# Kernel optimization log

Measured on AMD Instinct MI355X. Metric: run time of the kernel, lower is better.

Reference implementation:

```python
import jax, jax.numpy as jnp
import numpy as np

T, B = 1024, 64
IN, HID, OUT, ASZ = 512, 512, 512, 128


def lstm_cell(x, h, c, Wih, Whh, bih, bhh):
    g = x @ Wih.T + bih + h @ Whh.T + bhh
    i, f, gg, o = jnp.split(g, 4, axis=1)
    c2 = jax.nn.sigmoid(f) * c + jax.nn.sigmoid(i) * jnp.tanh(gg)
    h2 = jax.nn.sigmoid(o) * jnp.tanh(c2)
    return h2, c2


def arnn_cell(x, h, pol, Wih, Whh, b, ninp, nhid):
    # policy chunks: [ninp, nhid, nhid, nhid, nhid, nhid]
    p_in = pol[:, :ninp]
    p_h = pol[:, ninp:ninp + nhid]
    p_ig = pol[:, ninp + nhid:ninp + 2 * nhid]
    p_hg = pol[:, ninp + 2 * nhid:ninp + 3 * nhid]
    p_b = pol[:, ninp + 3 * nhid:ninp + 4 * nhid]
    ig = ((x * p_in) @ Wih.T) * p_ig + b * p_b
    hg = ((h * p_h) @ Whh.T) * p_hg
    return jnp.tanh(ig + hg)


def setup_inputs() -> dict:
    key = jax.random.key(0)
    ks = list(jax.random.split(key, 24))
    s = 0.1
    d = {"x": jax.random.normal(ks[0], (T, B, IN), dtype=jnp.float32)}
    # layer 0: ninp=IN, nhid=HID; layer 1: ninp=HID, nhid=OUT
    for l, (ninp, nhid) in enumerate([(IN, HID), (HID, OUT)]):
        ain = ASZ + ninp + nhid
        psz = ninp + 5 * nhid
        base = 1 + 9 * l
        d[f"aW_ih{l}"] = jax.random.normal(ks[base + 0], (4 * ASZ, ain)) * s
        d[f"aW_hh{l}"] = jax.random.normal(ks[base + 1], (4 * ASZ, ASZ)) * s
        d[f"ab_ih{l}"] = jax.random.normal(ks[base + 2], (4 * ASZ,)) * s
        d[f"ab_hh{l}"] = jax.random.normal(ks[base + 3], (4 * ASZ,)) * s
        d[f"pW{l}"] = jax.random.normal(ks[base + 4], (psz, ASZ)) * s
        d[f"pb{l}"] = jax.random.normal(ks[base + 5], (psz,)) * s
        d[f"fW_ih{l}"] = jax.random.normal(ks[base + 6], (nhid, ninp)) * s
        d[f"fW_hh{l}"] = jax.random.normal(ks[base + 7], (nhid, nhid)) * s
        d[f"fb{l}"] = jax.random.normal(ks[base + 8], (nhid,)) * s
    return d


def reference(x, aW_ih0, aW_hh0, ab_ih0, ab_hh0, pW0, pb0, fW_ih0, fW_hh0, fb0,
              aW_ih1, aW_hh1, ab_ih1, ab_hh1, pW1, pb1, fW_ih1, fW_hh1, fb1):
    zB = lambda n: jnp.zeros((B, n), dtype=x.dtype)
    init = (zB(ASZ), zB(ASZ), zB(ASZ), zB(ASZ), zB(HID), zB(OUT))

    def step(carry, xt):
        ahx0, ahc0, ahx1, ahc1, fhx0, fhx1 = carry
        # layer 0: adapt input = [x_t, fhx0, adapt_hx of layer -1 (= layer 1)]
        ax0 = jnp.concatenate([xt, fhx0, ahx1], axis=1)
        ahx0, ahc0 = lstm_cell(ax0, ahx0, ahc0, aW_ih0, aW_hh0, ab_ih0, ab_hh0)
        pol0 = ahx0 @ pW0.T + pb0
        fhx0 = arnn_cell(xt, fhx0, pol0, fW_ih0, fW_hh0, fb0, IN, HID)
        # layer 1
        ax1 = jnp.concatenate([fhx0, fhx1, ahx0], axis=1)
        ahx1, ahc1 = lstm_cell(ax1, ahx1, ahc1, aW_ih1, aW_hh1, ab_ih1, ab_hh1)
        pol1 = ahx1 @ pW1.T + pb1
        fhx1 = arnn_cell(fhx0, fhx1, pol1, fW_ih1, fW_hh1, fb1, HID, OUT)
        return (ahx0, ahc0, ahx1, ahc1, fhx0, fhx1), fhx1

    _, out = jax.lax.scan(step, init, x)  # out: [T, B, OUT]
    return out
```

## Files before the change

kernel.cpp:

```cpp
#include <hip/hip_runtime.h>

#define TT    1024
#define NTHR  512
#define NWG   256

#define XB_SZ  65536
#define XA0    0
#define XA1    2048
#define XF0    4096
#define XF1    12288
#define XP0    20480
#define XP1    40960
#define X_ZERO_END 20480

#define O_BARB (8 * XB_SZ)

__device__ __forceinline__ float sigm(float x) { return 1.f / (1.f + __expf(-x)); }

__device__ __forceinline__ float dot_ks(const float* __restrict__ a,
                                        const float* __restrict__ w,
                                        int nq, int ks) {
  float s0=0.f,s1=0.f,s2=0.f,s3=0.f;
  const float4* a4=(const float4*)a; const float4* w4=(const float4*)w;
  #pragma unroll 8
  for (int k = 0; k < nq; ++k) {
    int i4 = (k<<2) + ks;
    float4 av = a4[i4], wv = w4[i4];
    s0=fmaf(av.x,wv.x,s0); s1=fmaf(av.y,wv.y,s1);
    s2=fmaf(av.z,wv.z,s2); s3=fmaf(av.w,wv.w,s3);
  }
  return (s0+s1)+(s2+s3);
}
__device__ __forceinline__ float dot3_ks(const float* __restrict__ a,
                                         const float* __restrict__ pp,
                                         const float* __restrict__ w,
                                         int nq, int ks) {
  float s0=0.f,s1=0.f,s2=0.f,s3=0.f;
  const float4* a4=(const float4*)a; const float4* p4=(const float4*)pp;
  const float4* w4=(const float4*)w;
  #pragma unroll 8
  for (int k = 0; k < nq; ++k) {
    int i4 = (k<<2) + ks;
    float4 av = a4[i4], pv = p4[i4], wv = w4[i4];
    s0=fmaf(av.x*pv.x,wv.x,s0); s1=fmaf(av.y*pv.y,wv.y,s1);
    s2=fmaf(av.z*pv.z,wv.z,s2); s3=fmaf(av.w*pv.w,wv.w,s3);
  }
  return (s0+s1)+(s2+s3);
}
__device__ __forceinline__ float dot_full(const float* __restrict__ a,
                                          const float* __restrict__ w) {
  float s0=0.f,s1=0.f,s2=0.f,s3=0.f;
  const float4* a4=(const float4*)a; const float4* w4=(const float4*)w;
  #pragma unroll 8
  for (int k = 0; k < 32; ++k) {
    float4 av = a4[k], wv = w4[k];
    s0=fmaf(av.x,wv.x,s0); s1=fmaf(av.y,wv.y,s1);
    s2=fmaf(av.z,wv.z,s2); s3=fmaf(av.w,wv.w,s3);
  }
  return (s0+s1)+(s2+s3);
}

__device__ __forceinline__ void xbar(int* cnt, int* ep, int e, int tid) {
  __syncthreads();
  if (tid == 0) {
    int old = __hip_atomic_fetch_add(cnt, 1, __ATOMIC_RELAXED,
                                     __HIP_MEMORY_SCOPE_AGENT);
    if (old == e * 32 - 1)
      __hip_atomic_store(ep, e, __ATOMIC_RELAXED, __HIP_MEMORY_SCOPE_AGENT);
    while (__hip_atomic_load(ep, __ATOMIC_RELAXED,
                             __HIP_MEMORY_SCOPE_AGENT) < e)
      __builtin_amdgcn_s_sleep(1);
    (void)__hip_atomic_load(ep, __ATOMIC_ACQUIRE, __HIP_MEMORY_SCOPE_AGENT);
  }
  __syncthreads();
}

struct Params {
  const float* x;
  const float *aW_ih0, *aW_hh0, *ab_ih0, *ab_hh0, *pW0, *pb0, *fW_ih0, *fW_hh0, *fb0;
  const float *aW_ih1, *aW_hh1, *ab_ih1, *ab_hh1, *pW1, *pb1, *fW_ih1, *fW_hh1, *fb1;
  float* out;
  float* ws;
};

__global__ __launch_bounds__(NTHR, 1)
void arnn_kernel(Params p) {
  extern __shared__ float lds[];
  __shared__ int s_rank;
  const int tid = threadIdx.x;
  float* __restrict__ ws = p.ws;

  int xcd;
  asm volatile("s_getreg_b32 %0, hwreg(HW_REG_XCC_ID)" : "=s"(xcd));
  xcd &= 7;

  int* bar = (int*)(ws + O_BARB);
  if (tid == 0)
    s_rank = __hip_atomic_fetch_add(&bar[2048 + xcd], 1,
                                    __ATOMIC_RELAXED, __HIP_MEMORY_SCOPE_AGENT);
  __syncthreads();
  const int r = s_rank;
  int* cnt = &bar[xcd * 256];
  int* ep  = &bar[xcd * 256 + 64];

  float* xb = ws + (size_t)xcd * XB_SZ;
  const int b0 = xcd * 8;

  for (int i = r * NTHR + tid; i < X_ZERO_END; i += 32 * NTHR) xb[i] = 0.f;

  const int lane = tid & 63;
  const int ks   = tid & 3;
  const int jj = tid >> 7, blL = (tid >> 4) & 7, q = (tid >> 2) & 3;
  const int jL = r * 4 + jj;
  const bool cell = (tid & 15) == 0;
  const int c4 = tid >> 5, blA = (tid >> 2) & 7;
  const int cA = r * 16 + c4;
  const int nA = r * 80 + (tid >> 3), blP = tid & 7;
  const int nB = r * 80 + 64 + (tid >> 3);

  float bi0=0,bf0=0,bg0=0,bo0=0, bi1=0,bf1=0,bg1=0,bo1=0;
  if (cell) {
    bi0 = p.ab_ih0[0*128+jL] + p.ab_hh0[0*128+jL];
    bf0 = p.ab_ih0[1*128+jL] + p.ab_hh0[1*128+jL];
    bg0 = p.ab_ih0[2*128+jL] + p.ab_hh0[2*128+jL];
    bo0 = p.ab_ih0[3*128+jL] + p.ab_hh0[3*128+jL];
    bi1 = p.ab_ih1[0*128+jL] + p.ab_hh1[0*128+jL];
    bf1 = p.ab_ih1[1*128+jL] + p.ab_hh1[1*128+jL];
    bg1 = p.ab_ih1[2*128+jL] + p.ab_hh1[2*128+jL];
    bo1 = p.ab_ih1[3*128+jL] + p.ab_hh1[3*128+jL];
  }
  const float fb0c = p.fb0[cA], fb1c = p.fb1[cA];
  const float pb0a = p.pb0[nA], pb1a = p.pb1[nA];
  float pb0b = 0.f, pb1b = 0.f;
  if (tid < 128) { pb0b = p.pb0[nB]; pb1b = p.pb1[nB]; }

  const int rowL = q * 128 + jL;
  const float* wih0 = p.aW_ih0 + (size_t)rowL * 1152;
  const float* whh0 = p.aW_hh0 + (size_t)rowL * 128;
  const float* wih1 = p.aW_ih1 + (size_t)rowL * 1152;
  const float* whh1 = p.aW_hh1 + (size_t)rowL * 128;
  const float* fwi0 = p.fW_ih0 + (size_t)cA * 512;
  const float* fwh0 = p.fW_hh0 + (size_t)cA * 512;
  const float* fwi1 = p.fW_ih1 + (size_t)cA * 512;
  const float* fwh1 = p.fW_hh1 + (size_t)cA * 512;

  float creg0 = 0.f, creg1 = 0.f;

  int e = 1;
  xbar(cnt, ep, e, tid);

  for (int t = 0; t < TT; ++t) {
    const int old = t & 1, nw = old ^ 1;
    float* ahx0_o = xb + XA0 + old * 1024;
    float* ahx0_n = xb + XA0 + nw  * 1024;
    float* ahx1_o = xb + XA1 + old * 1024;
    float* ahx1_n = xb + XA1 + nw  * 1024;
    float* fhx0_o = xb + XF0 + old * 4096;
    float* fhx0_n = xb + XF0 + nw  * 4096;
    float* fhx1_o = xb + XF1 + old * 4096;
    float* fhx1_n = xb + XF1 + nw  * 4096;
    float* pol0   = xb + XP0;
    float* pol1   = xb + XP1;
    const float* xt = p.x + ((size_t)t * 64 + b0) * 512;

    {
      float s = dot_ks(xt     + blL * 512, wih0,        32, ks)
              + dot_ks(fhx0_o + blL * 512, wih0 + 512,  32, ks)
              + dot_ks(ahx1_o + blL * 128, wih0 + 1024,  8, ks)
              + dot_ks(ahx0_o + blL * 128, whh0,         8, ks);
      s += __shfl_xor(s, 1); s += __shfl_xor(s, 2);
      float gi = __shfl(s,(lane&48)+0),  gf = __shfl(s,(lane&48)+4);
      float gg = __shfl(s,(lane&48)+8),  go = __shfl(s,(lane&48)+12);
      if (cell) {
        gi += bi0; gf += bf0; gg += bg0; go += bo0;
        float c2 = sigm(gf) * creg0 + sigm(gi) * tanhf(gg);
        creg0 = c2;
        ahx0_n[blL * 128 + jL] = sigm(go) * tanhf(c2);
      }
    }
    ++e; xbar(cnt, ep, e, tid);

    {
      pol0[blP * 2560 + nA] = pb0a +
          dot_full(ahx0_n + blP * 128, p.pW0 + (size_t)nA * 128);
      if (tid < 128)
        pol0[blP * 2560 + nB] = pb0b +
            dot_full(ahx0_n + blP * 128, p.pW0 + (size_t)nB * 128);
    }
    ++e; xbar(cnt, ep, e, tid);

    {
      const float* pr = pol0 + blA * 2560;
      float sig = dot3_ks(xt     + blA * 512, pr,       fwi0, 32, ks);
      float shg = dot3_ks(fhx0_o + blA * 512, pr + 512, fwh0, 32, ks);
      sig += __shfl_xor(sig, 1); sig += __shfl_xor(sig, 2);
      shg += __shfl_xor(shg, 1); shg += __shfl_xor(shg, 2);
      if (ks == 0) {
        float v = tanhf(sig * pr[1024 + cA] + fb0c * pr[2048 + cA]
                      + shg * pr[1536 + cA]);
        fhx0_n[blA * 512 + cA] = v;
      }
    }
    ++e; xbar(cnt, ep, e, tid);

    {
      float s = dot_ks(fhx0_n + blL * 512, wih1,        32, ks)
              + dot_ks(fhx1_o + blL * 512, wih1 + 512,  32, ks)
              + dot_ks(ahx0_n + blL * 128, wih1 + 1024,  8, ks)
              + dot_ks(ahx1_o + blL * 128, whh1,         8, ks);
      s += __shfl_xor(s, 1); s += __shfl_xor(s, 2);
      float gi = __shfl(s,(lane&48)+0),  gf = __shfl(s,(lane&48)+4);
      float gg = __shfl(s,(lane&48)+8),  go = __shfl(s,(lane&48)+12);
      if (cell) {
        gi += bi1; gf += bf1; gg += bg1; go += bo1;
        float c2 = sigm(gf) * creg1 + sigm(gi) * tanhf(gg);
        creg1 = c2;
        ahx1_n[blL * 128 + jL] = sigm(go) * tanhf(c2);
      }
    }
    ++e; xbar(cnt, ep, e, tid);

    {
      pol1[blP * 2560 + nA] = pb1a +
          dot_full(ahx1_n + blP * 128, p.pW1 + (size_t)nA * 128);
      if (tid < 128)
        pol1[blP * 2560 + nB] = pb1b +
            dot_full(ahx1_n + blP * 128, p.pW1 + (size_t)nB * 128);
    }
    ++e; xbar(cnt, ep, e, tid);

    {
      const float* pr = pol1 + blA * 2560;
      float sig = dot3_ks(fhx0_n + blA * 512, pr,       fwi1, 32, ks);
      float shg = dot3_ks(fhx1_o + blA * 512, pr + 512, fwh1, 32, ks);
      sig += __shfl_xor(sig, 1); sig += __shfl_xor(sig, 2);
      shg += __shfl_xor(shg, 1); shg += __shfl_xor(shg, 2);
      if (ks == 0) {
        float v = tanhf(sig * pr[1024 + cA] + fb1c * pr[2048 + cA]
                      + shg * pr[1536 + cA]);
        fhx1_n[blA * 512 + cA] = v;
        p.out[((size_t)t * 64 + b0 + blA) * 512 + cA] = v;
      }
    }
    ++e; xbar(cnt, ep, e, tid);
  }
  (void)lds;
}

extern "C" void kernel_launch(void* const* d_in, const int* in_sizes, int n_in,
                              void* d_out, int out_size, void* d_ws, size_t ws_size,
                              hipStream_t stream) {
  Params prm;
  prm.x      = (const float*)d_in[0];
  prm.aW_ih0 = (const float*)d_in[1];
  prm.aW_hh0 = (const float*)d_in[2];
  prm.ab_ih0 = (const float*)d_in[3];
  prm.ab_hh0 = (const float*)d_in[4];
  prm.pW0    = (const float*)d_in[5];
  prm.pb0    = (const float*)d_in[6];
  prm.fW_ih0 = (const float*)d_in[7];
  prm.fW_hh0 = (const float*)d_in[8];
  prm.fb0    = (const float*)d_in[9];
  prm.aW_ih1 = (const float*)d_in[10];
  prm.aW_hh1 = (const float*)d_in[11];
  prm.ab_ih1 = (const float*)d_in[12];
  prm.ab_hh1 = (const float*)d_in[13];
  prm.pW1    = (const float*)d_in[14];
  prm.pb1    = (const float*)d_in[15];
  prm.fW_ih1 = (const float*)d_in[16];
  prm.fW_hh1 = (const float*)d_in[17];
  prm.fb1    = (const float*)d_in[18];
  prm.out    = (float*)d_out;
  prm.ws     = (float*)d_ws;

  hipMemsetAsync((char*)d_ws + (size_t)O_BARB * 4, 0, 16384, stream);

  static int lds_bytes = 84 * 1024;
  hipFuncSetAttribute((const void*)arnn_kernel,
                      hipFuncAttributeMaxDynamicSharedMemorySize, lds_bytes);

  void* kargs[] = { (void*)&prm };
  hipLaunchCooperativeKernel((const void*)arnn_kernel, dim3(NWG), dim3(NTHR),
                             kargs, lds_bytes, stream);
}
```

Baseline: 98.07 ms.

## Stage next phase's weights into double-buffered LDS overlapped with current compute

Each phase now issues global loads of the next phase's weight slice into registers, then computes from LDS, then writes the staged registers into the alternate LDS buffer before the grid barrier. Weight reads in the dot products come from padded LDS rows instead of global memory, and the global latency is hidden behind the current phase. This costs extra register pressure (nine float4 staging registers) and extra LDS write traffic on every phase, and the per-step weight reload from L2 still happens.

```diff
diff --git a/kernel.cpp b/kernel.cpp
--- a/kernel.cpp
+++ b/kernel.cpp
@@ -14,6 +14,8 @@
 #define X_ZERO_END 20480
 
 #define O_BARB (8 * XB_SZ)
+
+#define BUF_FL 18496
 
 __device__ __forceinline__ float sigm(float x) { return 1.f / (1.f + __expf(-x)); }
 
@@ -60,6 +62,60 @@
   return (s0+s1)+(s2+s3);
 }
 
+__device__ __forceinline__ void stg_lstm_ld(const float* Wih, int r, float4* st, int tid) {
+  const float4* g = (const float4*)Wih;
+  #pragma unroll
+  for (int k = 0; k < 9; ++k) {
+    int c = tid + k * 512;
+    int rr = c / 288, cq = c - rr * 288;
+    int grow = (rr >> 2) * 128 + r * 4 + (rr & 3);
+    st[k] = g[(size_t)grow * 288 + cq];
+  }
+}
+__device__ __forceinline__ void stg_lstm_wr(float* buf, const float4* st, int tid) {
+  #pragma unroll
+  for (int k = 0; k < 9; ++k) {
+    int c = tid + k * 512;
+    int rr = c / 288, cq = c - rr * 288;
+    *(float4*)(buf + rr * 1156 + cq * 4) = st[k];
+  }
+}
+__device__ __forceinline__ void stg_pol_ld(const float* pW, int r, float4* st, int tid) {
+  const float4* g = (const float4*)pW;
+  #pragma unroll
+  for (int k = 0; k < 5; ++k) {
+    int c = tid + k * 512;
+    int rw = c >> 5, cq = c & 31;
+    st[k] = g[(size_t)(r * 80 + rw) * 32 + cq];
+  }
+}
+__device__ __forceinline__ void stg_pol_wr(float* buf, const float4* st, int tid) {
+  #pragma unroll
+  for (int k = 0; k < 5; ++k) {
+    int c = tid + k * 512;
+    int rw = c >> 5, cq = c & 31;
+    *(float4*)(buf + rw * 132 + cq * 4) = st[k];
+  }
+}
+__device__ __forceinline__ void stg_arnn_ld(const float* Wih, const float* Whh,
+                                            int r, float4* st, int tid) {
+  #pragma unroll
+  for (int k = 0; k < 8; ++k) {
+    int c = tid + k * 512;
+    int rw = c >> 7, cq = c & 127;
+    const float4* g = (const float4*)((rw < 16) ? Wih : Whh);
+    st[k] = g[(size_t)(r * 16 + (rw & 15)) * 128 + cq];
+  }
+}
+__device__ __forceinline__ void stg_arnn_wr(float* buf, const float4* st, int tid) {
+  #pragma unroll
+  for (int k = 0; k < 8; ++k) {
+    int c = tid + k * 512;
+    int rw = c >> 7, cq = c & 127;
+    *(float4*)(buf + rw * 516 + cq * 4) = st[k];
+  }
+}
+
 __device__ __forceinline__ void xbar(int* cnt, int* ep, int e, int tid) {
   __syncthreads();
   if (tid == 0) {
@@ -115,8 +171,9 @@
   const bool cell = (tid & 15) == 0;
   const int c4 = tid >> 5, blA = (tid >> 2) & 7;
   const int cA = r * 16 + c4;
-  const int nA = r * 80 + (tid >> 3), blP = tid & 7;
-  const int nB = r * 80 + 64 + (tid >> 3);
+  const int nAr = tid >> 3, blP = tid & 7;
+  const int nA = r * 80 + nAr;
+  const int nB = r * 80 + 64 + nAr;
 
   float bi0=0,bf0=0,bg0=0,bo0=0, bi1=0,bf1=0,bg1=0,bo1=0;
   if (cell) {
@@ -135,16 +192,14 @@
   if (tid < 128) { pb0b = p.pb0[nB]; pb1b = p.pb1[nB]; }
 
   const int rowL = q * 128 + jL;
-  const float* wih0 = p.aW_ih0 + (size_t)rowL * 1152;
   const float* whh0 = p.aW_hh0 + (size_t)rowL * 128;
-  const float* wih1 = p.aW_ih1 + (size_t)rowL * 1152;
   const float* whh1 = p.aW_hh1 + (size_t)rowL * 128;
-  const float* fwi0 = p.fW_ih0 + (size_t)cA * 512;
-  const float* fwh0 = p.fW_hh0 + (size_t)cA * 512;
-  const float* fwi1 = p.fW_ih1 + (size_t)cA * 512;
-  const float* fwh1 = p.fW_hh1 + (size_t)cA * 512;
 
   float creg0 = 0.f, creg1 = 0.f;
+  float4 st[9];
+
+  stg_lstm_ld(p.aW_ih0, r, st, tid);
+  stg_lstm_wr(lds, st, tid);
 
   int e = 1;
   xbar(cnt, ep, e, tid);
@@ -163,11 +218,13 @@
     float* pol1   = xb + XP1;
     const float* xt = p.x + ((size_t)t * 64 + b0) * 512;
 
-    {
-      float s = dot_ks(xt     + blL * 512, wih0,        32, ks)
-              + dot_ks(fhx0_o + blL * 512, wih0 + 512,  32, ks)
-              + dot_ks(ahx1_o + blL * 128, wih0 + 1024,  8, ks)
-              + dot_ks(ahx0_o + blL * 128, whh0,         8, ks);
+    stg_pol_ld(p.pW0, r, st, tid);
+    {
+      const float* w = lds + (q * 4 + jj) * 1156;
+      float s = dot_ks(xt     + blL * 512, w,        32, ks)
+              + dot_ks(fhx0_o + blL * 512, w + 512,  32, ks)
+              + dot_ks(ahx1_o + blL * 128, w + 1024,  8, ks)
+              + dot_ks(ahx0_o + blL * 128, whh0,      8, ks);
       s += __shfl_xor(s, 1); s += __shfl_xor(s, 2);
       float gi = __shfl(s,(lane&48)+0),  gf = __shfl(s,(lane&48)+4);
       float gg = __shfl(s,(lane&48)+8),  go = __shfl(s,(lane&48)+12);
@@ -178,21 +235,26 @@
         ahx0_n[blL * 128 + jL] = sigm(go) * tanhf(c2);
       }
     }
-    ++e; xbar(cnt, ep, e, tid);
-
-    {
-      pol0[blP * 2560 + nA] = pb0a +
-          dot_full(ahx0_n + blP * 128, p.pW0 + (size_t)nA * 128);
+    stg_pol_wr(lds + BUF_FL, st, tid);
+    ++e; xbar(cnt, ep, e, tid);
+
+    stg_arnn_ld(p.fW_ih0, p.fW_hh0, r, st, tid);
+    {
+      const float* Lb = lds + BUF_FL;
+      pol0[blP * 2560 + nA] = pb0a + dot_full(ahx0_n + blP * 128, Lb + nAr * 132);
       if (tid < 128)
-        pol0[blP * 2560 + nB] = pb0b +
-            dot_full(ahx0_n + blP * 128, p.pW0 + (size_t)nB * 128);
-    }
-    ++e; xbar(cnt, ep, e, tid);
-
-    {
+        pol0[blP * 2560 + nB] = pb0b + dot_full(ahx0_n + blP * 128, Lb + (64 + nAr) * 132);
+    }
+    stg_arnn_wr(lds, st, tid);
+    ++e; xbar(cnt, ep, e, tid);
+
+    stg_lstm_ld(p.aW_ih1, r, st, tid);
+    {
+      const float* wi = lds + c4 * 516;
+      const float* wh = lds + (16 + c4) * 516;
       const float* pr = pol0 + blA * 2560;
-      float sig = dot3_ks(xt     + blA * 512, pr,       fwi0, 32, ks);
-      float shg = dot3_ks(fhx0_o + blA * 512, pr + 512, fwh0, 32, ks);
+      float sig = dot3_ks(xt     + blA * 512, pr,       wi, 32, ks);
+      float shg = dot3_ks(fhx0_o + blA * 512, pr + 512, wh, 32, ks);
       sig += __shfl_xor(sig, 1); sig += __shfl_xor(sig, 2);
       shg += __shfl_xor(shg, 1); shg += __shfl_xor(shg, 2);
       if (ks == 0) {
@@ -201,13 +263,16 @@
         fhx0_n[blA * 512 + cA] = v;
       }
     }
-    ++e; xbar(cnt, ep, e, tid);
-
-    {
-      float s = dot_ks(fhx0_n + blL * 512, wih1,        32, ks)
-              + dot_ks(fhx1_o + blL * 512, wih1 + 512,  32, ks)
-              + dot_ks(ahx0_n + blL * 128, wih1 + 1024,  8, ks)
-              + dot_ks(ahx1_o + blL * 128, whh1,         8, ks);
+    stg_lstm_wr(lds + BUF_FL, st, tid);
+    ++e; xbar(cnt, ep, e, tid);
+
+    stg_pol_ld(p.pW1, r, st, tid);
+    {
+      const float* w = lds + BUF_FL + (q * 4 + jj) * 1156;
+      float s = dot_ks(fhx0_n + blL * 512, w,        32, ks)
+              + dot_ks(fhx1_o + blL * 512, w + 512,  32, ks)
+              + dot_ks(ahx0_n + blL * 128, w + 1024,  8, ks)
+              + dot_ks(ahx1_o + blL * 128, whh1,      8, ks);
       s += __shfl_xor(s, 1); s += __shfl_xor(s, 2);
       float gi = __shfl(s,(lane&48)+0),  gf = __shfl(s,(lane&48)+4);
       float gg = __shfl(s,(lane&48)+8),  go = __shfl(s,(lane&48)+12);
@@ -218,21 +283,25 @@
         ahx1_n[blL * 128 + jL] = sigm(go) * tanhf(c2);
       }
     }
-    ++e; xbar(cnt, ep, e, tid);
-
-    {
-      pol1[blP * 2560 + nA] = pb1a +
-          dot_full(ahx1_n + blP * 128, p.pW1 + (size_t)nA * 128);
+    stg_pol_wr(lds, st, tid);
+    ++e; xbar(cnt, ep, e, tid);
+
+    stg_arnn_ld(p.fW_ih1, p.fW_hh1, r, st, tid);
+    {
+      pol1[blP * 2560 + nA] = pb1a + dot_full(ahx1_n + blP * 128, lds + nAr * 132);
       if (tid < 128)
-        pol1[blP * 2560 + nB] = pb1b +
-            dot_full(ahx1_n + blP * 128, p.pW1 + (size_t)nB * 128);
-    }
-    ++e; xbar(cnt, ep, e, tid);
-
-    {
+        pol1[blP * 2560 + nB] = pb1b + dot_full(ahx1_n + blP * 128, lds + (64 + nAr) * 132);
+    }
+    stg_arnn_wr(lds + BUF_FL, st, tid);
+    ++e; xbar(cnt, ep, e, tid);
+
+    stg_lstm_ld(p.aW_ih0, r, st, tid);
+    {
+      const float* wi = lds + BUF_FL + c4 * 516;
+      const float* wh = lds + BUF_FL + (16 + c4) * 516;
       const float* pr = pol1 + blA * 2560;
-      float sig = dot3_ks(fhx0_n + blA * 512, pr,       fwi1, 32, ks);
-      float shg = dot3_ks(fhx1_o + blA * 512, pr + 512, fwh1, 32, ks);
+      float sig = dot3_ks(fhx0_n + blA * 512, pr,       wi, 32, ks);
+      float shg = dot3_ks(fhx1_o + blA * 512, pr + 512, wh, 32, ks);
       sig += __shfl_xor(sig, 1); sig += __shfl_xor(sig, 2);
       shg += __shfl_xor(shg, 1); shg += __shfl_xor(shg, 2);
       if (ks == 0) {
@@ -242,9 +311,9 @@
         p.out[((size_t)t * 64 + b0 + blA) * 512 + cA] = v;
       }
     }
-    ++e; xbar(cnt, ep, e, tid);
-  }
-  (void)lds;
+    stg_lstm_wr(lds, st, tid);
+    ++e; xbar(cnt, ep, e, tid);
+  }
 }
 
 extern "C" void kernel_launch(void* const* d_in, const int* in_sizes, int n_in,
@@ -275,7 +344,7 @@
 
   hipMemsetAsync((char*)d_ws + (size_t)O_BARB * 4, 0, 16384, stream);
 
-  static int lds_bytes = 84 * 1024;
+  static int lds_bytes = 2 * BUF_FL * 4;
   hipFuncSetAttribute((const void*)arnn_kernel,
                       hipFuncAttributeMaxDynamicSharedMemorySize, lds_bytes);
 
```

Measured after the change: 133.8 ms. 36.4% more time.

## Prefetch next phase's weights into double-buffered LDS via async global-to-LDS loads

Applied to the files above, without the earlier changes.

Each phase now issues async global_load_lds copies of the weights the next phase needs (LSTM input weights, policy weights, ARNN weights) into one of two LDS slots. The copies run while the current phase computes against the other slot. Dot products then read weights from LDS, using an XOR swizzle to avoid bank conflicts, instead of from global memory. This hides weight-fetch latency behind compute and the grid barriers. It relies on the barriers' syncthreads to make the async loads visible, and there is no explicit vmcnt wait, which risks a race.

```diff
diff --git a/kernel.cpp b/kernel.cpp
--- a/kernel.cpp
+++ b/kernel.cpp
@@ -15,7 +15,15 @@
 
 #define O_BARB (8 * XB_SZ)
 
+#define SLOT_FL 18432
+
 __device__ __forceinline__ float sigm(float x) { return 1.f / (1.f + __expf(-x)); }
+
+__device__ __forceinline__ void gld_lds(const float* g, float* l) {
+  __builtin_amdgcn_global_load_lds(
+      (const __attribute__((address_space(1))) void*)g,
+      (__attribute__((address_space(3))) void*)l, 16, 0, 0);
+}
 
 __device__ __forceinline__ float dot_ks(const float* __restrict__ a,
                                         const float* __restrict__ w,
@@ -26,6 +34,21 @@
   for (int k = 0; k < nq; ++k) {
     int i4 = (k<<2) + ks;
     float4 av = a4[i4], wv = w4[i4];
+    s0=fmaf(av.x,wv.x,s0); s1=fmaf(av.y,wv.y,s1);
+    s2=fmaf(av.z,wv.z,s2); s3=fmaf(av.w,wv.w,s3);
+  }
+  return (s0+s1)+(s2+s3);
+}
+__device__ __forceinline__ float dot_lx(const float* __restrict__ a,
+                                        const float4* __restrict__ w4,
+                                        int nq, int ks, int xr) {
+  float s0=0.f,s1=0.f,s2=0.f,s3=0.f;
+  const float4* a4=(const float4*)a;
+  #pragma unroll 8
+  for (int k = 0; k < nq; ++k) {
+    int t = (k<<2) + ks;
+    float4 av = a4[t];
+    float4 wv = w4[t ^ xr];
     s0=fmaf(av.x,wv.x,s0); s1=fmaf(av.y,wv.y,s1);
     s2=fmaf(av.z,wv.z,s2); s3=fmaf(av.w,wv.w,s3);
   }
@@ -47,17 +70,55 @@
   }
   return (s0+s1)+(s2+s3);
 }
-__device__ __forceinline__ float dot_full(const float* __restrict__ a,
-                                          const float* __restrict__ w) {
+__device__ __forceinline__ float dot_pol(const float* __restrict__ a,
+                                         const float* __restrict__ w,
+                                         int xr) {
   float s0=0.f,s1=0.f,s2=0.f,s3=0.f;
   const float4* a4=(const float4*)a; const float4* w4=(const float4*)w;
   #pragma unroll 8
   for (int k = 0; k < 32; ++k) {
-    float4 av = a4[k], wv = w4[k];
+    float4 av = a4[k], wv = w4[k ^ xr];
     s0=fmaf(av.x,wv.x,s0); s1=fmaf(av.y,wv.y,s1);
     s2=fmaf(av.z,wv.z,s2); s3=fmaf(av.w,wv.w,s3);
   }
   return (s0+s1)+(s2+s3);
+}
+
+__device__ __forceinline__ void stage_lstm(const float* W, float* buf,
+                                           int r, int wv, int lane) {
+  #pragma unroll
+  for (int ci = 0; ci < 9; ++ci) {
+    int c = wv * 9 + ci;
+    int f4 = c * 64 + lane;
+    int rr = f4 / 288, sp = f4 - rr * 288;
+    int s  = sp ^ ((rr >> 2) << 1);
+    int grow = (rr >> 2) * 128 + r * 4 + (rr & 3);
+    gld_lds(W + ((size_t)grow * 288 + s) * 4, buf + (size_t)c * 256);
+  }
+}
+__device__ __forceinline__ void stage_pol(const float* pW, float* buf,
+                                          int r, int wv, int lane) {
+  #pragma unroll
+  for (int ci = 0; ci < 5; ++ci) {
+    int c = wv * 5 + ci;
+    int f4 = c * 64 + lane;
+    int nr = f4 >> 5, sp = f4 & 31;
+    int s  = sp ^ (nr & 7);
+    gld_lds(pW + ((size_t)(r * 80 + nr) * 32 + s) * 4, buf + (size_t)c * 256);
+  }
+}
+__device__ __forceinline__ void stage_arnn(const float* Wih, const float* Whh,
+                                           float* buf, int r, int wv, int lane) {
+  #pragma unroll
+  for (int ci = 0; ci < 8; ++ci) {
+    int c = wv * 8 + ci;
+    int f4 = c * 64 + lane;
+    int rw = f4 >> 7, cq = f4 & 127;
+    const float* g = (rw < 16)
+        ? Wih + ((size_t)(r * 16 + rw) * 128 + cq) * 4
+        : Whh + ((size_t)(r * 16 + rw - 16) * 128 + cq) * 4;
+    gld_lds(g, buf + (size_t)c * 256);
+  }
 }
 
 __device__ __forceinline__ void xbar(int* cnt, int* ep, int e, int tid) {
@@ -109,14 +170,16 @@
   for (int i = r * NTHR + tid; i < X_ZERO_END; i += 32 * NTHR) xb[i] = 0.f;
 
   const int lane = tid & 63;
+  const int wv   = tid >> 6;
   const int ks   = tid & 3;
   const int jj = tid >> 7, blL = (tid >> 4) & 7, q = (tid >> 2) & 3;
   const int jL = r * 4 + jj;
   const bool cell = (tid & 15) == 0;
   const int c4 = tid >> 5, blA = (tid >> 2) & 7;
   const int cA = r * 16 + c4;
-  const int nA = r * 80 + (tid >> 3), blP = tid & 7;
-  const int nB = r * 80 + 64 + (tid >> 3);
+  const int nAr = tid >> 3, blP = tid & 7;
+  const int nA = r * 80 + nAr;
+  const int nB = r * 80 + 64 + nAr;
 
   float bi0=0,bf0=0,bg0=0,bo0=0, bi1=0,bf1=0,bg1=0,bo1=0;
   if (cell) {
@@ -135,16 +198,17 @@
   if (tid < 128) { pb0b = p.pb0[nB]; pb1b = p.pb1[nB]; }
 
   const int rowL = q * 128 + jL;
-  const float* wih0 = p.aW_ih0 + (size_t)rowL * 1152;
   const float* whh0 = p.aW_hh0 + (size_t)rowL * 128;
-  const float* wih1 = p.aW_ih1 + (size_t)rowL * 1152;
   const float* whh1 = p.aW_hh1 + (size_t)rowL * 128;
-  const float* fwi0 = p.fW_ih0 + (size_t)cA * 512;
-  const float* fwh0 = p.fW_hh0 + (size_t)cA * 512;
-  const float* fwi1 = p.fW_ih1 + (size_t)cA * 512;
-  const float* fwh1 = p.fW_hh1 + (size_t)cA * 512;
+
+  float* slotA = lds;
+  float* slotB = lds + SLOT_FL;
+  const int xrL = q << 1;
+  const int xrP = nAr & 7;
 
   float creg0 = 0.f, creg1 = 0.f;
+
+  stage_lstm(p.aW_ih0, slotA, r, wv, lane);
 
   int e = 1;
   xbar(cnt, ep, e, tid);
@@ -163,11 +227,13 @@
     float* pol1   = xb + XP1;
     const float* xt = p.x + ((size_t)t * 64 + b0) * 512;
 
-    {
-      float s = dot_ks(xt     + blL * 512, wih0,        32, ks)
-              + dot_ks(fhx0_o + blL * 512, wih0 + 512,  32, ks)
-              + dot_ks(ahx1_o + blL * 128, wih0 + 1024,  8, ks)
-              + dot_ks(ahx0_o + blL * 128, whh0,         8, ks);
+    stage_pol(p.pW0, slotB, r, wv, lane);
+    {
+      const float4* Lr = (const float4*)(slotA + (q * 4 + jj) * 1152);
+      float s = dot_lx(xt     + blL * 512, Lr,        32, ks, xrL)
+              + dot_lx(fhx0_o + blL * 512, Lr + 128,  32, ks, xrL)
+              + dot_lx(ahx1_o + blL * 128, Lr + 256,   8, ks, xrL)
+              + dot_ks(ahx0_o + blL * 128, whh0,       8, ks);
       s += __shfl_xor(s, 1); s += __shfl_xor(s, 2);
       float gi = __shfl(s,(lane&48)+0),  gf = __shfl(s,(lane&48)+4);
       float gg = __shfl(s,(lane&48)+8),  go = __shfl(s,(lane&48)+12);
@@ -180,19 +246,23 @@
     }
     ++e; xbar(cnt, ep, e, tid);
 
+    stage_arnn(p.fW_ih0, p.fW_hh0, slotA, r, wv, lane);
     {
       pol0[blP * 2560 + nA] = pb0a +
-          dot_full(ahx0_n + blP * 128, p.pW0 + (size_t)nA * 128);
+          dot_pol(ahx0_n + blP * 128, slotB + nAr * 128, xrP);
       if (tid < 128)
         pol0[blP * 2560 + nB] = pb0b +
-            dot_full(ahx0_n + blP * 128, p.pW0 + (size_t)nB * 128);
-    }
-    ++e; xbar(cnt, ep, e, tid);
-
-    {
+            dot_pol(ahx0_n + blP * 128, slotB + (64 + nAr) * 128, xrP);
+    }
+    ++e; xbar(cnt, ep, e, tid);
+
+    stage_lstm(p.aW_ih1, slotB, r, wv, lane);
+    {
+      const float* wi = slotA + c4 * 512;
+      const float* wh = slotA + (16 + c4) * 512;
       const float* pr = pol0 + blA * 2560;
-      float sig = dot3_ks(xt     + blA * 512, pr,       fwi0, 32, ks);
-      float shg = dot3_ks(fhx0_o + blA * 512, pr + 512, fwh0, 32, ks);
+      float sig = dot3_ks(xt     + blA * 512, pr,       wi, 32, ks);
+      float shg = dot3_ks(fhx0_o + blA * 512, pr + 512, wh, 32, ks);
       sig += __shfl_xor(sig, 1); sig += __shfl_xor(sig, 2);
       shg += __shfl_xor(shg, 1); shg += __shfl_xor(shg, 2);
       if (ks == 0) {
@@ -203,11 +273,13 @@
     }
     ++e; xbar(cnt, ep, e, tid);
 
-    {
-      float s = dot_ks(fhx0_n + blL * 512, wih1,        32, ks)
-              + dot_ks(fhx1_o + blL * 512, wih1 + 512,  32, ks)
-              + dot_ks(ahx0_n + blL * 128, wih1 + 1024,  8, ks)
-              + dot_ks(ahx1_o + blL * 128, whh1,         8, ks);
+    stage_pol(p.pW1, slotA, r, wv, lane);
+    {
+      const float4* Lr = (const float4*)(slotB + (q * 4 + jj) * 1152);
+      float s = dot_lx(fhx0_n + blL * 512, Lr,        32, ks, xrL)
+              + dot_lx(fhx1_o + blL * 512, Lr + 128,  32, ks, xrL)
+              + dot_lx(ahx0_n + blL * 128, Lr + 256,   8, ks, xrL)
+              + dot_ks(ahx1_o + blL * 128, whh1,       8, ks);
       s += __shfl_xor(s, 1); s += __shfl_xor(s, 2);
       float gi = __shfl(s,(lane&48)+0),  gf = __shfl(s,(lane&48)+4);
       float gg = __shfl(s,(lane&48)+8),  go = __shfl(s,(lane&48)+12);
@@ -220,19 +292,23 @@
     }
     ++e; xbar(cnt, ep, e, tid);
 
+    stage_arnn(p.fW_ih1, p.fW_hh1, slotB, r, wv, lane);
     {
       pol1[blP * 2560 + nA] = pb1a +
-          dot_full(ahx1_n + blP * 128, p.pW1 + (size_t)nA * 128);
+          dot_pol(ahx1_n + blP * 128, slotA + nAr * 128, xrP);
       if (tid < 128)
         pol1[blP * 2560 + nB] = pb1b +
-            dot_full(ahx1_n + blP * 128, p.pW1 + (size_t)nB * 128);
-    }
-    ++e; xbar(cnt, ep, e, tid);
-
-    {
+            dot_pol(ahx1_n + blP * 128, slotA + (64 + nAr) * 128, xrP);
+    }
+    ++e; xbar(cnt, ep, e, tid);
+
+    stage_lstm(p.aW_ih0, slotA, r, wv, lane);
+    {
+      const float* wi = slotB + c4 * 512;
+      const float* wh = slotB + (16 + c4) * 512;
       const float* pr = pol1 + blA * 2560;
-      float sig = dot3_ks(fhx0_n + blA * 512, pr,       fwi1, 32, ks);
-      float shg = dot3_ks(fhx1_o + blA * 512, pr + 512, fwh1, 32, ks);
+      float sig = dot3_ks(fhx0_n + blA * 512, pr,       wi, 32, ks);
+      float shg = dot3_ks(fhx1_o + blA * 512, pr + 512, wh, 32, ks);
       sig += __shfl_xor(sig, 1); sig += __shfl_xor(sig, 2);
       shg += __shfl_xor(shg, 1); shg += __shfl_xor(shg, 2);
       if (ks == 0) {
@@ -244,7 +320,6 @@
     }
     ++e; xbar(cnt, ep, e, tid);
   }
-  (void)lds;
 }
 
 extern "C" void kernel_launch(void* const* d_in, const int* in_sizes, int n_in,
@@ -275,7 +350,7 @@
 
   hipMemsetAsync((char*)d_ws + (size_t)O_BARB * 4, 0, 16384, stream);
 
-  static int lds_bytes = 84 * 1024;
+  static int lds_bytes = 2 * SLOT_FL * 4;
   hipFuncSetAttribute((const void*)arnn_kernel,
                       hipFuncAttributeMaxDynamicSharedMemorySize, lds_bytes);
 
```

Result: slower. 118.9 ms (+21.3%).

## Replace counter barrier with per-rank flag barrier and relaxed atomic loads of shared state

Applied to the files above, without the earlier changes.

Replaces the atomic-counter plus epoch barrier with a flag array: each workgroup stores its epoch to its own flag, and thread 0 polls all 32 flags of its XCD group. Reads of cross-workgroup state (hidden states, policy vectors) now go through relaxed agent-scope atomic loads instead of plain loads, and the acquire fence in the barrier is dropped. The aim is to remove atomic RMW contention and the acquire cost on every barrier. In exchange each poll issues 32 loads, and the atomic loads are 64-bit rather than 128-bit vector loads, which may cost bandwidth.

```diff
diff --git a/kernel.cpp b/kernel.cpp
--- a/kernel.cpp
+++ b/kernel.cpp
@@ -17,6 +17,16 @@
 
 __device__ __forceinline__ float sigm(float x) { return 1.f / (1.f + __expf(-x)); }
 
+__device__ __forceinline__ float ald(const float* p) {
+  return __hip_atomic_load(p, __ATOMIC_RELAXED, __HIP_MEMORY_SCOPE_AGENT);
+}
+__device__ __forceinline__ float2 ald2(const float* p) {
+  unsigned long long v = __hip_atomic_load((const unsigned long long*)p,
+      __ATOMIC_RELAXED, __HIP_MEMORY_SCOPE_AGENT);
+  return make_float2(__uint_as_float((unsigned)v),
+                     __uint_as_float((unsigned)(v >> 32)));
+}
+
 __device__ __forceinline__ float dot_ks(const float* __restrict__ a,
                                         const float* __restrict__ w,
                                         int nq, int ks) {
@@ -31,46 +41,83 @@
   }
   return (s0+s1)+(s2+s3);
 }
-__device__ __forceinline__ float dot3_ks(const float* __restrict__ a,
-                                         const float* __restrict__ pp,
+__device__ __forceinline__ float dotA_ks(const float* a,
                                          const float* __restrict__ w,
                                          int nq, int ks) {
   float s0=0.f,s1=0.f,s2=0.f,s3=0.f;
-  const float4* a4=(const float4*)a; const float4* p4=(const float4*)pp;
   const float4* w4=(const float4*)w;
   #pragma unroll 8
   for (int k = 0; k < nq; ++k) {
     int i4 = (k<<2) + ks;
-    float4 av = a4[i4], pv = p4[i4], wv = w4[i4];
-    s0=fmaf(av.x*pv.x,wv.x,s0); s1=fmaf(av.y*pv.y,wv.y,s1);
-    s2=fmaf(av.z*pv.z,wv.z,s2); s3=fmaf(av.w*pv.w,wv.w,s3);
-  }
-  return (s0+s1)+(s2+s3);
-}
-__device__ __forceinline__ float dot_full(const float* __restrict__ a,
-                                          const float* __restrict__ w) {
+    float2 a0 = ald2(a + i4*4), a1 = ald2(a + i4*4 + 2);
+    float4 wv = w4[i4];
+    s0=fmaf(a0.x,wv.x,s0); s1=fmaf(a0.y,wv.y,s1);
+    s2=fmaf(a1.x,wv.z,s2); s3=fmaf(a1.y,wv.w,s3);
+  }
+  return (s0+s1)+(s2+s3);
+}
+__device__ __forceinline__ float dot3X_ks(const float* __restrict__ a,
+                                          const float* pp,
+                                          const float* __restrict__ w,
+                                          int nq, int ks) {
   float s0=0.f,s1=0.f,s2=0.f,s3=0.f;
   const float4* a4=(const float4*)a; const float4* w4=(const float4*)w;
   #pragma unroll 8
+  for (int k = 0; k < nq; ++k) {
+    int i4 = (k<<2) + ks;
+    float4 av = a4[i4], wv = w4[i4];
+    float2 p0 = ald2(pp + i4*4), p1 = ald2(pp + i4*4 + 2);
+    s0=fmaf(av.x*p0.x,wv.x,s0); s1=fmaf(av.y*p0.y,wv.y,s1);
+    s2=fmaf(av.z*p1.x,wv.z,s2); s3=fmaf(av.w*p1.y,wv.w,s3);
+  }
+  return (s0+s1)+(s2+s3);
+}
+__device__ __forceinline__ float dot3A_ks(const float* a, const float* pp,
+                                          const float* __restrict__ w,
+                                          int nq, int ks) {
+  float s0=0.f,s1=0.f,s2=0.f,s3=0.f;
+  const float4* w4=(const float4*)w;
+  #pragma unroll 8
+  for (int k = 0; k < nq; ++k) {
+    int i4 = (k<<2) + ks;
+    float2 a0 = ald2(a + i4*4), a1 = ald2(a + i4*4 + 2);
+    float2 p0 = ald2(pp + i4*4), p1 = ald2(pp + i4*4 + 2);
+    float4 wv = w4[i4];
+    s0=fmaf(a0.x*p0.x,wv.x,s0); s1=fmaf(a0.y*p0.y,wv.y,s1);
+    s2=fmaf(a1.x*p1.x,wv.z,s2); s3=fmaf(a1.y*p1.y,wv.w,s3);
+  }
+  return (s0+s1)+(s2+s3);
+}
+__device__ __forceinline__ float dotA_full(const float* a,
+                                           const float* __restrict__ w) {
+  float s0=0.f,s1=0.f,s2=0.f,s3=0.f;
+  const float4* w4=(const float4*)w;
+  #pragma unroll 8
   for (int k = 0; k < 32; ++k) {
-    float4 av = a4[k], wv = w4[k];
-    s0=fmaf(av.x,wv.x,s0); s1=fmaf(av.y,wv.y,s1);
-    s2=fmaf(av.z,wv.z,s2); s3=fmaf(av.w,wv.w,s3);
-  }
-  return (s0+s1)+(s2+s3);
-}
-
-__device__ __forceinline__ void xbar(int* cnt, int* ep, int e, int tid) {
+    float2 a0 = ald2(a + k*4), a1 = ald2(a + k*4 + 2);
+    float4 wv = w4[k];
+    s0=fmaf(a0.x,wv.x,s0); s1=fmaf(a0.y,wv.y,s1);
+    s2=fmaf(a1.x,wv.z,s2); s3=fmaf(a1.y,wv.w,s3);
+  }
+  return (s0+s1)+(s2+s3);
+}
+
+__device__ __forceinline__ void xbar(int* flags, int r, int e, int tid) {
   __syncthreads();
   if (tid == 0) {
-    int old = __hip_atomic_fetch_add(cnt, 1, __ATOMIC_RELAXED,
-                                     __HIP_MEMORY_SCOPE_AGENT);
-    if (old == e * 32 - 1)
-      __hip_atomic_store(ep, e, __ATOMIC_RELAXED, __HIP_MEMORY_SCOPE_AGENT);
-    while (__hip_atomic_load(ep, __ATOMIC_RELAXED,
-                             __HIP_MEMORY_SCOPE_AGENT) < e)
+    __hip_atomic_store(&flags[r], e, __ATOMIC_RELAXED, __HIP_MEMORY_SCOPE_AGENT);
+    for (;;) {
+      bool ok = true;
+      #pragma unroll
+      for (int i = 0; i < 32; ++i) {
+        int v = __hip_atomic_load(&flags[i], __ATOMIC_RELAXED,
+                                  __HIP_MEMORY_SCOPE_AGENT);
+        ok &= (v >= e);
+      }
+      if (ok) break;
       __builtin_amdgcn_s_sleep(1);
-    (void)__hip_atomic_load(ep, __ATOMIC_ACQUIRE, __HIP_MEMORY_SCOPE_AGENT);
+    }
+    asm volatile("" ::: "memory");
   }
   __syncthreads();
 }
@@ -96,12 +143,11 @@
 
   int* bar = (int*)(ws + O_BARB);
   if (tid == 0)
-    s_rank = __hip_atomic_fetch_add(&bar[2048 + xcd], 1,
+    s_rank = __hip_atomic_fetch_add(&bar[1024 + xcd], 1,
                                     __ATOMIC_RELAXED, __HIP_MEMORY_SCOPE_AGENT);
   __syncthreads();
   const int r = s_rank;
-  int* cnt = &bar[xcd * 256];
-  int* ep  = &bar[xcd * 256 + 64];
+  int* flags = &bar[xcd * 64];
 
   float* xb = ws + (size_t)xcd * XB_SZ;
   const int b0 = xcd * 8;
@@ -115,8 +161,9 @@
   const bool cell = (tid & 15) == 0;
   const int c4 = tid >> 5, blA = (tid >> 2) & 7;
   const int cA = r * 16 + c4;
-  const int nA = r * 80 + (tid >> 3), blP = tid & 7;
-  const int nB = r * 80 + 64 + (tid >> 3);
+  const int nAr = tid >> 3, blP = tid & 7;
+  const int nA = r * 80 + nAr;
+  const int nB = r * 80 + 64 + nAr;
 
   float bi0=0,bf0=0,bg0=0,bo0=0, bi1=0,bf1=0,bg1=0,bo1=0;
   if (cell) {
@@ -147,7 +194,7 @@
   float creg0 = 0.f, creg1 = 0.f;
 
   int e = 1;
-  xbar(cnt, ep, e, tid);
+  xbar(flags, r, e, tid);
 
   for (int t = 0; t < TT; ++t) {
     const int old = t & 1, nw = old ^ 1;
@@ -164,10 +211,10 @@
     const float* xt = p.x + ((size_t)t * 64 + b0) * 512;
 
     {
-      float s = dot_ks(xt     + blL * 512, wih0,        32, ks)
-              + dot_ks(fhx0_o + blL * 512, wih0 + 512,  32, ks)
-              + dot_ks(ahx1_o + blL * 128, wih0 + 1024,  8, ks)
-              + dot_ks(ahx0_o + blL * 128, whh0,         8, ks);
+      float s = dot_ks (xt     + blL * 512, wih0,        32, ks)
+              + dotA_ks(fhx0_o + blL * 512, wih0 + 512,  32, ks)
+              + dotA_ks(ahx1_o + blL * 128, wih0 + 1024,  8, ks)
+              + dotA_ks(ahx0_o + blL * 128, whh0,         8, ks);
       s += __shfl_xor(s, 1); s += __shfl_xor(s, 2);
       float gi = __shfl(s,(lane&48)+0),  gf = __shfl(s,(lane&48)+4);
       float gg = __shfl(s,(lane&48)+8),  go = __shfl(s,(lane&48)+12);
@@ -178,36 +225,36 @@
         ahx0_n[blL * 128 + jL] = sigm(go) * tanhf(c2);
       }
     }
-    ++e; xbar(cnt, ep, e, tid);
+    ++e; xbar(flags, r, e, tid);
 
     {
       pol0[blP * 2560 + nA] = pb0a +
-          dot_full(ahx0_n + blP * 128, p.pW0 + (size_t)nA * 128);
+          dotA_full(ahx0_n + blP * 128, p.pW0 + (size_t)nA * 128);
       if (tid < 128)
         pol0[blP * 2560 + nB] = pb0b +
-            dot_full(ahx0_n + blP * 128, p.pW0 + (size_t)nB * 128);
-    }
-    ++e; xbar(cnt, ep, e, tid);
+            dotA_full(ahx0_n + blP * 128, p.pW0 + (size_t)nB * 128);
+    }
+    ++e; xbar(flags, r, e, tid);
 
     {
       const float* pr = pol0 + blA * 2560;
-      float sig = dot3_ks(xt     + blA * 512, pr,       fwi0, 32, ks);
-      float shg = dot3_ks(fhx0_o + blA * 512, pr + 512, fwh0, 32, ks);
+      float sig = dot3X_ks(xt     + blA * 512, pr,       fwi0, 32, ks);
+      float shg = dot3A_ks(fhx0_o + blA * 512, pr + 512, fwh0, 32, ks);
       sig += __shfl_xor(sig, 1); sig += __shfl_xor(sig, 2);
       shg += __shfl_xor(shg, 1); shg += __shfl_xor(shg, 2);
       if (ks == 0) {
-        float v = tanhf(sig * pr[1024 + cA] + fb0c * pr[2048 + cA]
-                      + shg * pr[1536 + cA]);
+        float v = tanhf(sig * ald(pr + 1024 + cA) + fb0c * ald(pr + 2048 + cA)
+                      + shg * ald(pr + 1536 + cA));
         fhx0_n[blA * 512 + cA] = v;
       }
     }
-    ++e; xbar(cnt, ep, e, tid);
-
-    {
-      float s = dot_ks(fhx0_n + blL * 512, wih1,        32, ks)
-              + dot_ks(fhx1_o + blL * 512, wih1 + 512,  32, ks)
-              + dot_ks(ahx0_n + blL * 128, wih1 + 1024,  8, ks)
-              + dot_ks(ahx1_o + blL * 128, whh1,         8, ks);
+    ++e; xbar(flags, r, e, tid);
+
+    {
+      float s = dotA_ks(fhx0_n + blL * 512, wih1,        32, ks)
+              + dotA_ks(fhx1_o + blL * 512, wih1 + 512,  32, ks)
+              + dotA_ks(ahx0_n + blL * 128, wih1 + 1024,  8, ks)
+              + dotA_ks(ahx1_o + blL * 128, whh1,         8, ks);
       s += __shfl_xor(s, 1); s += __shfl_xor(s, 2);
       float gi = __shfl(s,(lane&48)+0),  gf = __shfl(s,(lane&48)+4);
       float gg = __shfl(s,(lane&48)+8),  go = __shfl(s,(lane&48)+12);
@@ -218,31 +265,31 @@
         ahx1_n[blL * 128 + jL] = sigm(go) * tanhf(c2);
       }
     }
-    ++e; xbar(cnt, ep, e, tid);
+    ++e; xbar(flags, r, e, tid);
 
     {
       pol1[blP * 2560 + nA] = pb1a +
-          dot_full(ahx1_n + blP * 128, p.pW1 + (size_t)nA * 128);
+          dotA_full(ahx1_n + blP * 128, p.pW1 + (size_t)nA * 128);
       if (tid < 128)
         pol1[blP * 2560 + nB] = pb1b +
-            dot_full(ahx1_n + blP * 128, p.pW1 + (size_t)nB * 128);
-    }
-    ++e; xbar(cnt, ep, e, tid);
+            dotA_full(ahx1_n + blP * 128, p.pW1 + (size_t)nB * 128);
+    }
+    ++e; xbar(flags, r, e, tid);
 
     {
       const float* pr = pol1 + blA * 2560;
-      float sig = dot3_ks(fhx0_n + blA * 512, pr,       fwi1, 32, ks);
-      float shg = dot3_ks(fhx1_o + blA * 512, pr + 512, fwh1, 32, ks);
+      float sig = dot3A_ks(fhx0_n + blA * 512, pr,       fwi1, 32, ks);
+      float shg = dot3A_ks(fhx1_o + blA * 512, pr + 512, fwh1, 32, ks);
       sig += __shfl_xor(sig, 1); sig += __shfl_xor(sig, 2);
       shg += __shfl_xor(shg, 1); shg += __shfl_xor(shg, 2);
       if (ks == 0) {
-        float v = tanhf(sig * pr[1024 + cA] + fb1c * pr[2048 + cA]
-                      + shg * pr[1536 + cA]);
+        float v = tanhf(sig * ald(pr + 1024 + cA) + fb1c * ald(pr + 2048 + cA)
+                      + shg * ald(pr + 1536 + cA));
         fhx1_n[blA * 512 + cA] = v;
         p.out[((size_t)t * 64 + b0 + blA) * 512 + cA] = v;
       }
     }
-    ++e; xbar(cnt, ep, e, tid);
+    ++e; xbar(flags, r, e, tid);
   }
   (void)lds;
 }
@@ -273,7 +320,7 @@
   prm.out    = (float*)d_out;
   prm.ws     = (float*)d_ws;
 
-  hipMemsetAsync((char*)d_ws + (size_t)O_BARB * 4, 0, 16384, stream);
+  hipMemsetAsync((char*)d_ws + (size_t)O_BARB * 4, 0, 8192, stream);
 
   static int lds_bytes = 84 * 1024;
   hipFuncSetAttribute((const void*)arnn_kernel,
```

Measured after the change: 172.1 ms. 1.75x slower.
